# Performance work log

Hardware: AMD Instinct MI355X
Metric: run time of the kernel (lower is better)

Reference implementation:

```python
import jax, jax.numpy as jnp
import numpy as np

B, H, S, D = 16, 12, 1024, 64  # batch, heads, seq, head_dim (dim=768, num_head=12)


def setup_inputs() -> dict:
    key = jax.random.key(0)
    ks = jax.random.split(key, 9)
    sc = 1.0 / np.sqrt(D)
    return {
        "x": jax.random.normal(ks[0], (B, H, S, D), dtype=jnp.float32),
        "Wq": jax.random.normal(ks[1], (D, D), dtype=jnp.float32) * sc,
        "bq": jax.random.normal(ks[2], (D,), dtype=jnp.float32) * 0.02,
        "Wk": jax.random.normal(ks[3], (D, D), dtype=jnp.float32) * sc,
        "bk": jax.random.normal(ks[4], (D,), dtype=jnp.float32) * 0.02,
        "Wv": jax.random.normal(ks[5], (D, D), dtype=jnp.float32) * sc,
        "bv": jax.random.normal(ks[6], (D,), dtype=jnp.float32) * 0.02,
        "Wo": jax.random.normal(ks[7], (D, D), dtype=jnp.float32) * sc,
        "bo": jax.random.normal(ks[8], (D,), dtype=jnp.float32) * 0.02,
    }


def reference(x, Wq, bq, Wk, bk, Wv, bv, Wo, bo):
    # torch Linear: y = x @ W^T + b, applied to last dim (head_dim)
    q = jnp.einsum("bhsd,ed->bhse", x, Wq) + bq
    k = jnp.einsum("bhsd,ed->bhse", x, Wk) + bk
    v = jnp.einsum("bhsd,ed->bhse", x, Wv) + bv
    scores = jnp.einsum("bhqd,bhkd->bhqk", q, k) / jnp.sqrt(jnp.float32(q.shape[-1]))
    attn = jax.nn.softmax(scores, axis=-1)
    out = jnp.einsum("bhqk,bhkd->bhqd", attn, v)
    out = jnp.einsum("bhsd,ed->bhse", out, Wo) + bo
    return out
```

## Files before the change

### kernel.cpp

```cpp
#include <hip/hip_runtime.h>
#include <math.h>


typedef __bf16 bf16x8 __attribute__((ext_vector_type(8)));
typedef float  f32x4  __attribute__((ext_vector_type(4)));

#define MFMA(a, b, c) __builtin_amdgcn_mfma_f32_16x16x32_bf16((a), (b), (c), 0, 0, 0)

static constexpr int S = 1024;
static constexpr int PAD = 72;
static constexpr size_t NE = 196608ull * 64ull;
static constexpr float QSCALE = 0.125f * 1.4426950408889634f;

__device__ inline unsigned long long pack4bf(float a, float b, float c, float d) {
    union { __bf16 h[4]; unsigned long long u; } pk;
    pk.h[0] = (__bf16)a; pk.h[1] = (__bf16)b; pk.h[2] = (__bf16)c; pk.h[3] = (__bf16)d;
    return pk.u;
}

union frag_u { bf16x8 v; unsigned long long u[2]; };

__global__ __launch_bounds__(256, 3) void projkv(
    const float* __restrict__ x,
    const float* __restrict__ Wk, const float* __restrict__ bk,
    const float* __restrict__ Wv, const float* __restrict__ bv,
    __bf16* __restrict__ gk, __bf16* __restrict__ gvt)
{
    __shared__ __align__(16) __bf16 lx[128][PAD];
    __shared__ __align__(16) __bf16 lbuf[128][PAD];
    __shared__ __align__(16) __bf16 lw[2][8][64][8];
    __shared__ float lb[2][64];

    const int tid = threadIdx.x;
    const int row_base = blockIdx.x * 128;

    #pragma unroll
    for (int i = tid * 4; i < 8192; i += 1024) {
        float4 v = *(const float4*)(x + (size_t)row_base * 64 + i);
        int r = i >> 6, c = i & 63;
        *(unsigned long long*)&lx[r][c] = pack4bf(v.x, v.y, v.z, v.w);
    }
    #pragma unroll
    for (int c = tid; c < 1024; c += 256) {
        int mtx = c >> 9, rest = c & 511;
        int fe = rest >> 6, ln = rest & 63;
        int mm = ln & 15, qq = ln >> 4;
        int et = fe >> 1, half = fe & 1;
        const float* src = (mtx ? Wv : Wk) + (size_t)(et * 16 + mm) * 64 + half * 32 + qq * 8;
        float4 u0 = *(const float4*)(src);
        float4 u1 = *(const float4*)(src + 4);
        *(unsigned long long*)&lw[mtx][fe][ln][0] = pack4bf(u0.x, u0.y, u0.z, u0.w);
        *(unsigned long long*)&lw[mtx][fe][ln][4] = pack4bf(u1.x, u1.y, u1.z, u1.w);
    }
    if (tid < 64) { lb[0][tid] = bk[tid]; lb[1][tid] = bv[tid]; }
    __syncthreads();

    const int w = tid >> 6, lane = tid & 63, m = lane & 15, quad = lane >> 4;
    const int bh = row_base >> 10;
    const int s_base = row_base & 1023;

    bf16x8 xf[2][2];
    #pragma unroll
    for (int g = 0; g < 2; g++) {
        xf[g][0] = *(const bf16x8*)&lx[w * 32 + g * 16 + m][quad * 8];
        xf[g][1] = *(const bf16x8*)&lx[w * 32 + g * 16 + m][32 + quad * 8];
    }

    #pragma unroll
    for (int et = 0; et < 4; et++) {
        bf16x8 wf0 = *(const bf16x8*)&lw[0][et * 2 + 0][lane][0];
        bf16x8 wf1 = *(const bf16x8*)&lw[0][et * 2 + 1][lane][0];
        float4 bias = *(const float4*)&lb[0][et * 16 + quad * 4];
        #pragma unroll
        for (int g = 0; g < 2; g++) {
            f32x4 acc = {0.f, 0.f, 0.f, 0.f};
            acc = MFMA(wf0, xf[g][0], acc);
            acc = MFMA(wf1, xf[g][1], acc);
            *(unsigned long long*)&lbuf[w * 32 + g * 16 + m][et * 16 + quad * 4] =
                pack4bf(acc[0] + bias.x, acc[1] + bias.y,
                        acc[2] + bias.z, acc[3] + bias.w);
        }
    }
    __syncthreads();
    #pragma unroll
    for (int it = 0; it < 4; it++) {
        int idx = it * 256 + tid;
        int row = idx >> 3, col = (idx & 7) * 8;
        *(uint4*)(gk + ((size_t)row_base + row) * 64 + col) = *(uint4*)&lbuf[row][col];
    }
    __syncthreads();

    __bf16 (*lvt)[136] = (__bf16(*)[136])&lbuf[0][0];
    #pragma unroll
    for (int et = 0; et < 4; et++) {
        bf16x8 wf0 = *(const bf16x8*)&lw[1][et * 2 + 0][lane][0];
        bf16x8 wf1 = *(const bf16x8*)&lw[1][et * 2 + 1][lane][0];
        const float bias = lb[1][et * 16 + m];
        #pragma unroll
        for (int g = 0; g < 2; g++) {
            f32x4 acc = {0.f, 0.f, 0.f, 0.f};
            acc = MFMA(xf[g][0], wf0, acc);
            acc = MFMA(xf[g][1], wf1, acc);
            const int tp = (2 * w + g) & 3;
            const int p0 = 64 * (w >> 1) + 32 * (tp >> 1) + 8 * quad + 4 * (tp & 1);
            *(unsigned long long*)&lvt[et * 16 + m][p0] =
                pack4bf(acc[0] + bias, acc[1] + bias, acc[2] + bias, acc[3] + bias);
        }
    }
    __syncthreads();
    #pragma unroll
    for (int it = 0; it < 4; it++) {
        int idx = it * 256 + tid;
        int row = idx >> 4, col = (idx & 15) * 8;
        *(uint4*)(gvt + ((size_t)bh * 64 + row) * 1024 + s_base + col) = *(uint4*)&lvt[row][col];
    }
}

__global__ __launch_bounds__(512, 4) void attn(
    const float* __restrict__ x,
    const float* __restrict__ Wq, const float* __restrict__ bq,
    const __bf16* __restrict__ gk, const __bf16* __restrict__ gvt,
    const float* __restrict__ Wo, const float* __restrict__ bo,
    float* __restrict__ out)
{
    __shared__ __align__(16) union {
        __bf16 xq[256][PAD];
        struct {
            __bf16 k[64][PAD];
            __bf16 v[64][PAD];
        } m;
    } L;

    const int tid = threadIdx.x;
    const int w = tid >> 6, lane = tid & 63, m = lane & 15, quad = lane >> 4;
    const int bh = blockIdx.x;
    const int q0 = blockIdx.y * 256 + w * 32;

    const float* xq32 = x + ((size_t)bh * 1024 + blockIdx.y * 256) * 64;
    #pragma unroll
    for (int i = tid * 4; i < 16384; i += 2048) {
        float4 v = *(const float4*)(xq32 + i);
        int r = i >> 6, c = i & 63;
        *(unsigned long long*)&L.xq[r][c] = pack4bf(v.x, v.y, v.z, v.w);
    }
    __syncthreads();

    bf16x8 xqf[2][2];
    #pragma unroll
    for (int g = 0; g < 2; g++) {
        xqf[g][0] = *(const bf16x8*)&L.xq[w * 32 + g * 16 + m][quad * 8];
        xqf[g][1] = *(const bf16x8*)&L.xq[w * 32 + g * 16 + m][32 + quad * 8];
    }
    #pragma unroll
    for (int et = 0; et < 4; et++) {
        const float* wqrow = Wq + (size_t)(et * 16 + m) * 64;
        float4 a0 = *(const float4*)(wqrow + quad * 8);
        float4 a1 = *(const float4*)(wqrow + quad * 8 + 4);
        float4 a2 = *(const float4*)(wqrow + 32 + quad * 8);
        float4 a3 = *(const float4*)(wqrow + 36 + quad * 8);
        frag_u wf0, wf1;
        wf0.u[0] = pack4bf(a0.x, a0.y, a0.z, a0.w);
        wf0.u[1] = pack4bf(a1.x, a1.y, a1.z, a1.w);
        wf1.u[0] = pack4bf(a2.x, a2.y, a2.z, a2.w);
        wf1.u[1] = pack4bf(a3.x, a3.y, a3.z, a3.w);
        float4 bias = *(const float4*)(bq + et * 16 + quad * 4);
        #pragma unroll
        for (int g = 0; g < 2; g++) {
            f32x4 acc = {0.f, 0.f, 0.f, 0.f};
            acc = MFMA(wf0.v, xqf[g][0], acc);
            acc = MFMA(wf1.v, xqf[g][1], acc);
            *(unsigned long long*)&L.xq[w * 32 + g * 16 + m][et * 16 + quad * 4] =
                pack4bf((acc[0] + bias.x) * QSCALE, (acc[1] + bias.y) * QSCALE,
                        (acc[2] + bias.z) * QSCALE, (acc[3] + bias.w) * QSCALE);
        }
    }
    bf16x8 qf[2][2];
    #pragma unroll
    for (int g = 0; g < 2; g++) {
        qf[g][0] = *(const bf16x8*)&L.xq[w * 32 + g * 16 + m][quad * 8];
        qf[g][1] = *(const bf16x8*)&L.xq[w * 32 + g * 16 + m][32 + quad * 8];
    }

    const int sr = tid >> 3;
    const int sc = (tid & 7) * 8;
    const __bf16* kbase = gk + (size_t)bh * S * 64;
    const __bf16* vbase = gvt + (size_t)bh * 64 * 1024;

    uint4 kreg = *(const uint4*)(kbase + (size_t)sr * 64 + sc);
    uint4 vreg = *(const uint4*)(vbase + (size_t)sr * 1024 + sc);

    __syncthreads();

    f32x4 o[2][4];
    float lsum[2] = {0.f, 0.f};
    #pragma unroll
    for (int g = 0; g < 2; g++)
        #pragma unroll
        for (int n = 0; n < 4; n++) o[g][n] = {0.f, 0.f, 0.f, 0.f};

    for (int kb = 0; kb < 16; kb++) {
        __syncthreads();
        *(uint4*)&L.m.k[sr][sc] = kreg;
        *(uint4*)&L.m.v[sr][sc] = vreg;
        if (kb < 15) {
            const int nb = (kb + 1) * 64;
            kreg = *(const uint4*)(kbase + (size_t)(nb + sr) * 64 + sc);
            vreg = *(const uint4*)(vbase + (size_t)sr * 1024 + nb + sc);
        }
        __syncthreads();

        __builtin_amdgcn_s_setprio(1);
        frag_u pb[2][2];
        #pragma unroll
        for (int t = 0; t < 4; t++) {
            bf16x8 ka0 = *(const bf16x8*)&L.m.k[t * 16 + m][quad * 8];
            bf16x8 ka1 = *(const bf16x8*)&L.m.k[t * 16 + m][32 + quad * 8];
            #pragma unroll
            for (int g = 0; g < 2; g++) {
                f32x4 acc = {0.f, 0.f, 0.f, 0.f};
                acc = MFMA(ka0, qf[g][0], acc);
                acc = MFMA(ka1, qf[g][1], acc);
                float e0 = __builtin_amdgcn_exp2f(acc[0]);
                float e1 = __builtin_amdgcn_exp2f(acc[1]);
                float e2 = __builtin_amdgcn_exp2f(acc[2]);
                float e3 = __builtin_amdgcn_exp2f(acc[3]);
                lsum[g] += (e0 + e1) + (e2 + e3);
                pb[g][t >> 1].u[t & 1] = pack4bf(e0, e1, e2, e3);
            }
        }
        #pragma unroll
        for (int n = 0; n < 4; n++) {
            bf16x8 va0 = *(const bf16x8*)&L.m.v[n * 16 + m][quad * 8];
            bf16x8 va1 = *(const bf16x8*)&L.m.v[n * 16 + m][32 + quad * 8];
            #pragma unroll
            for (int g = 0; g < 2; g++) {
                o[g][n] = MFMA(va0, pb[g][0].v, o[g][n]);
                o[g][n] = MFMA(va1, pb[g][1].v, o[g][n]);
            }
        }
        __builtin_amdgcn_s_setprio(0);
    }

    #pragma unroll
    for (int g = 0; g < 2; g++) {
        lsum[g] += __shfl_xor(lsum[g], 16);
        lsum[g] += __shfl_xor(lsum[g], 32);
    }

    bf16x8 wf[4][2];
    #pragma unroll
    for (int et = 0; et < 4; et++) {
        const float* worow = Wo + (size_t)(et * 16 + m) * 64;
        float4 c0 = *(const float4*)(worow + 4 * quad);
        float4 c1 = *(const float4*)(worow + 16 + 4 * quad);
        float4 c2 = *(const float4*)(worow + 32 + 4 * quad);
        float4 c3 = *(const float4*)(worow + 48 + 4 * quad);
        frag_u f0, f1;
        f0.u[0] = pack4bf(c0.x, c0.y, c0.z, c0.w);
        f0.u[1] = pack4bf(c1.x, c1.y, c1.z, c1.w);
        f1.u[0] = pack4bf(c2.x, c2.y, c2.z, c2.w);
        f1.u[1] = pack4bf(c3.x, c3.y, c3.z, c3.w);
        wf[et][0] = f0.v;
        wf[et][1] = f1.v;
    }
    float biasr[4];
    #pragma unroll
    for (int et = 0; et < 4; et++) biasr[et] = bo[et * 16 + m];

    #pragma unroll
    for (int g = 0; g < 2; g++) {
        const float inv = 1.f / lsum[g];
        frag_u af0, af1;
        af0.u[0] = pack4bf(o[g][0][0] * inv, o[g][0][1] * inv, o[g][0][2] * inv, o[g][0][3] * inv);
        af0.u[1] = pack4bf(o[g][1][0] * inv, o[g][1][1] * inv, o[g][1][2] * inv, o[g][1][3] * inv);
        af1.u[0] = pack4bf(o[g][2][0] * inv, o[g][2][1] * inv, o[g][2][2] * inv, o[g][2][3] * inv);
        af1.u[1] = pack4bf(o[g][3][0] * inv, o[g][3][1] * inv, o[g][3][2] * inv, o[g][3][3] * inv);
        #pragma unroll
        for (int et = 0; et < 4; et++) {
            f32x4 acc = {0.f, 0.f, 0.f, 0.f};
            acc = MFMA(af0.v, wf[et][0], acc);
            acc = MFMA(af1.v, wf[et][1], acc);
            #pragma unroll
            for (int r = 0; r < 4; r++) {
                size_t row = (size_t)bh * S + q0 + g * 16 + quad * 4 + r;
                out[row * 64 + et * 16 + m] = acc[r] + biasr[et];
            }
        }
    }
}

extern "C" void kernel_launch(void* const* d_in, const int* in_sizes, int n_in,
                              void* d_out, int out_size, void* d_ws, size_t ws_size,
                              hipStream_t stream) {
    const float* x  = (const float*)d_in[0];
    const float* Wq = (const float*)d_in[1];
    const float* bq = (const float*)d_in[2];
    const float* Wk = (const float*)d_in[3];
    const float* bk = (const float*)d_in[4];
    const float* Wv = (const float*)d_in[5];
    const float* bv = (const float*)d_in[6];
    const float* Wo = (const float*)d_in[7];
    const float* bo = (const float*)d_in[8];
    float* out = (float*)d_out;

    __bf16* gk  = (__bf16*)d_ws;
    __bf16* gvt = gk + NE;

    projkv<<<1536, 256, 0, stream>>>(x, Wk, bk, Wv, bv, gk, gvt);
    attn<<<dim3(192, 4), 512, 0, stream>>>(x, Wq, bq, gk, gvt, Wo, bo, out);
}
```

Measured before the change: 197.7 us.

## Software-pipeline attention loop with triple-buffered K/V in LDS

K/V tiles in shared memory become triple-buffered, and the main loop is restructured so the PV MFMAs for the previous key block are interleaved with the QK^T and exp work for the current block. This cuts the barriers to one per iteration and lets matrix and exp work from adjacent blocks overlap, adding a prologue and epilogue. The cost is a larger shared-memory union, about 55 KB instead of about 37 KB per block, which can lower the number of resident 512-thread blocks per CU below the launch-bounds target.

```diff
diff --git a/kernel.cpp b/kernel.cpp
--- a/kernel.cpp
+++ b/kernel.cpp
@@ -126,8 +126,8 @@
     __shared__ __align__(16) union {
         __bf16 xq[256][PAD];
         struct {
-            __bf16 k[64][PAD];
-            __bf16 v[64][PAD];
+            __bf16 k[3][64][PAD];
+            __bf16 v[3][64][PAD];
         } m;
     } L;
 
@@ -198,23 +198,62 @@
         #pragma unroll
         for (int n = 0; n < 4; n++) o[g][n] = {0.f, 0.f, 0.f, 0.f};
 
-    for (int kb = 0; kb < 16; kb++) {
+    *(uint4*)&L.m.k[0][sr][sc] = kreg;
+    *(uint4*)&L.m.v[0][sr][sc] = vreg;
+    kreg = *(const uint4*)(kbase + (size_t)(64 + sr) * 64 + sc);
+    vreg = *(const uint4*)(vbase + (size_t)sr * 1024 + 64 + sc);
+    __syncthreads();
+
+    *(uint4*)&L.m.k[1][sr][sc] = kreg;
+    *(uint4*)&L.m.v[1][sr][sc] = vreg;
+    kreg = *(const uint4*)(kbase + (size_t)(128 + sr) * 64 + sc);
+    vreg = *(const uint4*)(vbase + (size_t)sr * 1024 + 128 + sc);
+
+    frag_u pb[2][2];
+    __builtin_amdgcn_s_setprio(1);
+    #pragma unroll
+    for (int tn = 0; tn < 4; tn++) {
+        bf16x8 ka0 = *(const bf16x8*)&L.m.k[0][tn * 16 + m][quad * 8];
+        bf16x8 ka1 = *(const bf16x8*)&L.m.k[0][tn * 16 + m][32 + quad * 8];
+        #pragma unroll
+        for (int g = 0; g < 2; g++) {
+            f32x4 acc = {0.f, 0.f, 0.f, 0.f};
+            acc = MFMA(ka0, qf[g][0], acc);
+            acc = MFMA(ka1, qf[g][1], acc);
+            float e0 = __builtin_amdgcn_exp2f(acc[0]);
+            float e1 = __builtin_amdgcn_exp2f(acc[1]);
+            float e2 = __builtin_amdgcn_exp2f(acc[2]);
+            float e3 = __builtin_amdgcn_exp2f(acc[3]);
+            lsum[g] += (e0 + e1) + (e2 + e3);
+            pb[g][tn >> 1].u[tn & 1] = pack4bf(e0, e1, e2, e3);
+        }
+    }
+    __builtin_amdgcn_s_setprio(0);
+
+    int cur = 1, prv = 0, nxt = 2;
+    for (int kb = 1; kb < 15; kb++) {
         __syncthreads();
-        *(uint4*)&L.m.k[sr][sc] = kreg;
-        *(uint4*)&L.m.v[sr][sc] = vreg;
-        if (kb < 15) {
-            const int nb = (kb + 1) * 64;
+        *(uint4*)&L.m.k[nxt][sr][sc] = kreg;
+        *(uint4*)&L.m.v[nxt][sr][sc] = vreg;
+        if (kb < 14) {
+            const int nb = (kb + 2) * 64;
             kreg = *(const uint4*)(kbase + (size_t)(nb + sr) * 64 + sc);
             vreg = *(const uint4*)(vbase + (size_t)sr * 1024 + nb + sc);
         }
-        __syncthreads();
 
         __builtin_amdgcn_s_setprio(1);
-        frag_u pb[2][2];
-        #pragma unroll
-        for (int t = 0; t < 4; t++) {
-            bf16x8 ka0 = *(const bf16x8*)&L.m.k[t * 16 + m][quad * 8];
-            bf16x8 ka1 = *(const bf16x8*)&L.m.k[t * 16 + m][32 + quad * 8];
+        frag_u pbn[2][2];
+        #pragma unroll
+        for (int tn = 0; tn < 4; tn++) {
+            bf16x8 ka0 = *(const bf16x8*)&L.m.k[cur][tn * 16 + m][quad * 8];
+            bf16x8 ka1 = *(const bf16x8*)&L.m.k[cur][tn * 16 + m][32 + quad * 8];
+            bf16x8 va0 = *(const bf16x8*)&L.m.v[prv][tn * 16 + m][quad * 8];
+            bf16x8 va1 = *(const bf16x8*)&L.m.v[prv][tn * 16 + m][32 + quad * 8];
+            #pragma unroll
+            for (int g = 0; g < 2; g++) {
+                o[g][tn] = MFMA(va0, pb[g][0].v, o[g][tn]);
+                o[g][tn] = MFMA(va1, pb[g][1].v, o[g][tn]);
+            }
             #pragma unroll
             for (int g = 0; g < 2; g++) {
                 f32x4 acc = {0.f, 0.f, 0.f, 0.f};
@@ -225,17 +264,56 @@
                 float e2 = __builtin_amdgcn_exp2f(acc[2]);
                 float e3 = __builtin_amdgcn_exp2f(acc[3]);
                 lsum[g] += (e0 + e1) + (e2 + e3);
-                pb[g][t >> 1].u[t & 1] = pack4bf(e0, e1, e2, e3);
-            }
-        }
-        #pragma unroll
-        for (int n = 0; n < 4; n++) {
-            bf16x8 va0 = *(const bf16x8*)&L.m.v[n * 16 + m][quad * 8];
-            bf16x8 va1 = *(const bf16x8*)&L.m.v[n * 16 + m][32 + quad * 8];
-            #pragma unroll
-            for (int g = 0; g < 2; g++) {
-                o[g][n] = MFMA(va0, pb[g][0].v, o[g][n]);
-                o[g][n] = MFMA(va1, pb[g][1].v, o[g][n]);
+                pbn[g][tn >> 1].u[tn & 1] = pack4bf(e0, e1, e2, e3);
+            }
+        }
+        __builtin_amdgcn_s_setprio(0);
+        #pragma unroll
+        for (int g = 0; g < 2; g++)
+            #pragma unroll
+            for (int i = 0; i < 2; i++) {
+                pb[g][i].u[0] = pbn[g][i].u[0];
+                pb[g][i].u[1] = pbn[g][i].u[1];
+            }
+        int t = prv; prv = cur; cur = nxt; nxt = t;
+    }
+
+    __syncthreads();
+    {
+        __builtin_amdgcn_s_setprio(1);
+        frag_u pbn[2][2];
+        #pragma unroll
+        for (int tn = 0; tn < 4; tn++) {
+            bf16x8 ka0 = *(const bf16x8*)&L.m.k[cur][tn * 16 + m][quad * 8];
+            bf16x8 ka1 = *(const bf16x8*)&L.m.k[cur][tn * 16 + m][32 + quad * 8];
+            bf16x8 va0 = *(const bf16x8*)&L.m.v[prv][tn * 16 + m][quad * 8];
+            bf16x8 va1 = *(const bf16x8*)&L.m.v[prv][tn * 16 + m][32 + quad * 8];
+            #pragma unroll
+            for (int g = 0; g < 2; g++) {
+                o[g][tn] = MFMA(va0, pb[g][0].v, o[g][tn]);
+                o[g][tn] = MFMA(va1, pb[g][1].v, o[g][tn]);
+            }
+            #pragma unroll
+            for (int g = 0; g < 2; g++) {
+                f32x4 acc = {0.f, 0.f, 0.f, 0.f};
+                acc = MFMA(ka0, qf[g][0], acc);
+                acc = MFMA(ka1, qf[g][1], acc);
+                float e0 = __builtin_amdgcn_exp2f(acc[0]);
+                float e1 = __builtin_amdgcn_exp2f(acc[1]);
+                float e2 = __builtin_amdgcn_exp2f(acc[2]);
+                float e3 = __builtin_amdgcn_exp2f(acc[3]);
+                lsum[g] += (e0 + e1) + (e2 + e3);
+                pbn[g][tn >> 1].u[tn & 1] = pack4bf(e0, e1, e2, e3);
+            }
+        }
+        #pragma unroll
+        for (int tn = 0; tn < 4; tn++) {
+            bf16x8 va0 = *(const bf16x8*)&L.m.v[cur][tn * 16 + m][quad * 8];
+            bf16x8 va1 = *(const bf16x8*)&L.m.v[cur][tn * 16 + m][32 + quad * 8];
+            #pragma unroll
+            for (int g = 0; g < 2; g++) {
+                o[g][tn] = MFMA(va0, pbn[g][0].v, o[g][tn]);
+                o[g][tn] = MFMA(va1, pbn[g][1].v, o[g][tn]);
             }
         }
         __builtin_amdgcn_s_setprio(0);
```

New measurement: 198.3 us. Within noise of the previous version (+0.3%).
